# Optimization experiments

Measured on AMD Instinct MI355X. Metric: run time of the kernel, lower is better.

## Reference

```python
import jax, jax.numpy as jnp
from jax import lax
import numpy as np

EPS_COS = 1e-8   # cosine-similarity eps (matches F.cosine_similarity default scale)
EPS_IN = 1e-5    # InstanceNorm2d default eps
NEG = -1e9


def _conv3(x, w, b):
    # x: [B,C,H,W], w: [O,I,3,3]
    y = lax.conv_general_dilated(x, w, (1, 1), 'SAME',
                                 dimension_numbers=('NCHW', 'OIHW', 'NCHW'))
    return y + b[None, :, None, None]


def _inorm(x):
    m = jnp.mean(x, axis=(2, 3), keepdims=True)
    v = jnp.var(x, axis=(2, 3), keepdims=True)
    return (x - m) * lax.rsqrt(v + EPS_IN)


def _shift(former, latter, mask):
    # former/latter: [B,C,H,W]; mask: [H,W] int (1 = hole).
    # For every masked pixel, find the most cosine-similar UNMASKED pixel in the
    # latter (known-region encoder) features and copy the former feature from it.
    B, C, H, W = former.shape
    L = H * W
    lat = lax.stop_gradient(latter).reshape(B, C, L)           # attention is non-differentiable
    latn = lat / (jnp.linalg.norm(lat, axis=1, keepdims=True) + EPS_COS)
    sim = jnp.einsum('bcm,bcn->bmn', latn, latn)               # [B,L,L] query m -> key n
    mflat = mask.reshape(L) > 0
    sim = jnp.where(mflat[None, None, :], NEG, sim)            # keys must be unmasked
    idx = jnp.argmax(sim, axis=-1)                             # [B,L]
    fflat = former.reshape(B, C, L)
    gathered = jnp.take_along_axis(fflat, jnp.broadcast_to(idx[:, None, :], (B, C, L)), axis=2)
    shift = jnp.where(mflat[None, None, :], gathered, 0.0)     # zeros outside the hole
    return shift.reshape(B, C, H, W)


def setup_inputs() -> dict:
    key = jax.random.key(0)
    ks = jax.random.split(key, 6)
    B, C, H, W = 8, 256, 64, 64
    inp = jax.random.normal(ks[0], (B, 2 * C, H, W), dtype=jnp.float32)
    mask = jax.random.randint(ks[1], (H, W), 0, 2, dtype=jnp.int32)
    s1 = 1.0 / float(np.sqrt(2 * C * 9))
    s2 = 1.0 / float(np.sqrt(C * 9))
    W1 = jax.random.uniform(ks[2], (C, 2 * C, 3, 3), jnp.float32, -s1, s1)
    b1 = jax.random.uniform(ks[3], (C,), jnp.float32, -s1, s1)
    W2 = jax.random.uniform(ks[4], (C, C, 3, 3), jnp.float32, -s2, s2)
    b2 = jax.random.uniform(ks[5], (C,), jnp.float32, -s2, s2)
    return {"input": inp, "mask": mask, "W1": W1, "b1": b1, "W2": W2, "b2": b2}


def reference(input, mask, W1, b1, W2, b2):
    C = input.shape[1] // 2
    F_c = input[:, :C]          # former (decoder) features
    F_s = input[:, C:]          # latter (encoder) features
    F_shift = _shift(F_c, F_s, mask)
    F_fuse = F_c * F_shift
    F_com = jnp.concatenate([F_c, F_fuse], axis=1)             # [B,2C,H,W]
    h = jax.nn.relu(_inorm(_conv3(F_com, W1, b1)))
    res = _inorm(_conv3(h, W2, b2))
    return jnp.concatenate([F_c + res, F_s], axis=1)
```

## Files before the change

### kernel.cpp

```cpp
#include <hip/hip_runtime.h>
#include <hip/hip_bf16.h>
#include <math.h>

#define L 4096
#define C 256
#define B 8

typedef __attribute__((ext_vector_type(8))) short bf16x8;
typedef __attribute__((ext_vector_type(8))) ushort u16x8;
typedef __attribute__((ext_vector_type(4))) float f32x4;

__device__ inline ushort f2bu(float f) { __hip_bfloat16 h = __float2bfloat16(f); return *(ushort*)&h; }
__device__ inline float bu2f(ushort u) { __hip_bfloat16 h; *(ushort*)&h = u; return __bfloat162float(h); }

#define SWZ(c) ((((c) >> 1) & 3) << 4)

__global__ __launch_bounds__(256) void compact_mask(
    const int* __restrict__ mask, int* __restrict__ counts,
    int* __restrict__ maskedOrig, int* __restrict__ unmaskOrig,
    int* __restrict__ posOf)
{
    __shared__ int smM[256], smU[256];
    int t = threadIdx.x;
    int flags[16];
    int cm = 0, cu = 0;
    for (int k = 0; k < 16; ++k) {
        int l = t * 16 + k;
        int f = mask[l] > 0;
        flags[k] = f;
        cm += f; cu += !f;
    }
    smM[t] = cm; smU[t] = cu;
    __syncthreads();
    for (int off = 1; off < 256; off <<= 1) {
        int vM = 0, vU = 0;
        if (t >= off) { vM = smM[t - off]; vU = smU[t - off]; }
        __syncthreads();
        smM[t] += vM; smU[t] += vU;
        __syncthreads();
    }
    if (t == 255) { counts[0] = smM[255]; counts[1] = smU[255]; }
    int pm = smM[t] - cm, pu = smU[t] - cu;
    for (int k = 0; k < 16; ++k) {
        int l = t * 16 + k;
        if (flags[k]) { maskedOrig[pm] = l; posOf[l] = pm; pm++; }
        else          { unmaskOrig[pu] = l; posOf[l] = pu; pu++; }
    }
}

__global__ __launch_bounds__(256) void norm_transpose(
    const float* __restrict__ input, const int* __restrict__ mask,
    const int* __restrict__ counts, const int* __restrict__ posOf,
    ushort* __restrict__ fsnh, ushort* __restrict__ fsnl)
{
    int bx = blockIdx.x;
    int b = bx >> 7;
    int l0 = (bx & 127) * 32;
    __shared__ float tile[256 * 33];
    __shared__ float part[8 * 33];
    __shared__ float denom[32];
    __shared__ int   rowdst[32];
    int t = threadIdx.x;
    int lsub = t & 31, cg = t >> 5;
    for (int cc = 0; cc < 256; cc += 8) {
        int c = cc + cg;
        tile[c * 33 + lsub] = input[((size_t)(b * 512 + 256 + c)) * L + l0 + lsub];
    }
    __syncthreads();
    float s = 0.f;
    for (int c = cg; c < 256; c += 8) { float v = tile[c * 33 + lsub]; s = fmaf(v, v, s); }
    part[cg * 33 + lsub] = s;
    __syncthreads();
    if (t < 32) {
        float s2 = 0.f;
        for (int g = 0; g < 8; ++g) s2 += part[g * 33 + t];
        denom[t] = sqrtf(s2) + 1e-8f;
        int l = l0 + t;
        int Nm = counts[0];
        rowdst[t] = (mask[l] > 0) ? posOf[l] : (Nm + posOf[l]);
    }
    __syncthreads();
    for (int ls = 0; ls < 32; ++ls) {
        int r = rowdst[ls];
        float d = denom[ls];
        float val = tile[t * 33 + ls] / d;
        ushort h = f2bu(val);
        float hf = bu2f(h);
        ushort lo = f2bu(val - hf);
        size_t o = ((size_t)b * L + r) * C + t;
        fsnh[o] = h;
        fsnl[o] = lo;
    }
}

__global__ __launch_bounds__(256, 2) void sim_argmax_v8(
    const ushort* __restrict__ hi, const ushort* __restrict__ lo,
    const int* __restrict__ counts,
    float* __restrict__ pval, int* __restrict__ pidx)
{
    __shared__ ushort ldsB[32768];
    const int Nm = counts[0], Nu = counts[1];
    const int b = blockIdx.z;
    const int m0 = blockIdx.y * 64;
    const int half = blockIdx.x;
    const int t = threadIdx.x;
    const int w = t >> 6, l = t & 63;
    const int lm = l & 15, lk = l >> 4;
    const int key = lm << 4;

    const int nct = (Nu + 31) >> 5;
    const int hs = (nct + 1) >> 1;
    const int cA = half * hs, cB = half ? nct : hs;

    float bestv[4]; int bestn[4];
#pragma unroll
    for (int r = 0; r < 4; ++r) { bestv[r] = -3e38f; bestn[r] = 0; }

    if (m0 < Nm && cA < cB) {
        const char* bytesH = (const char*)hi;
        const char* bytesL = (const char*)lo;
        const size_t bL = (size_t)b * L;
        char* ldsc = (char*)ldsB;

#define STAGE(bofs, cc) do { \
    size_t gb = (bL + (size_t)Nm + (size_t)(cc) * 32) * 512; \
    _Pragma("unroll") \
    for (int i = 0; i < 4; ++i) { \
        int x = i * 4096 + t * 16; \
        int sx = x ^ (((x >> 9) & 15) << 4); \
        __builtin_amdgcn_global_load_lds((const __attribute__((address_space(1))) unsigned*)(bytesH + gb + sx), \
            (__attribute__((address_space(3))) unsigned*)(ldsc + (bofs) + x), 16, 0, 0); \
        __builtin_amdgcn_global_load_lds((const __attribute__((address_space(1))) unsigned*)(bytesL + gb + sx), \
            (__attribute__((address_space(3))) unsigned*)(ldsc + (bofs) + 16384 + x), 16, 0, 0); \
    } \
} while (0)

        STAGE(0, cA);
        if (cA + 1 < cB) STAGE(32768, cA + 1);

        const int rA = m0 + w * 16 + lm;
        bf16x8 ah[8], al[8];
        {
            const ushort* aH = hi + (bL + rA) * C + lk * 8;
            const ushort* aL = lo + (bL + rA) * C + lk * 8;
#pragma unroll
            for (int ks = 0; ks < 8; ++ks) {
                ah[ks] = *(const bf16x8*)(aH + ks * 32);
                al[ks] = *(const bf16x8*)(aL + ks * 32);
            }
        }

        for (int c = cA; c < cB; ++c) {
            int bob = ((c - cA) & 1) * 32768;
            if (c + 1 < cB) asm volatile("s_waitcnt vmcnt(8)" ::: "memory");
            else            asm volatile("s_waitcnt vmcnt(0)" ::: "memory");
            __builtin_amdgcn_s_barrier();
            const char* cbase = ldsc + bob;
            f32x4 acc[2];
            acc[0] = (f32x4){0.f, 0.f, 0.f, 0.f};
            acc[1] = (f32x4){0.f, 0.f, 0.f, 0.f};
#pragma unroll
            for (int ks = 0; ks < 8; ++ks) {
                bf16x8 bh[2], bl[2];
#pragma unroll
                for (int nf = 0; nf < 2; ++nf) {
                    int addr = (nf * 16 + lm) * 512 + ((ks * 64 + lk * 16) ^ key);
                    bh[nf] = *(const bf16x8*)(cbase + addr);
                    bl[nf] = *(const bf16x8*)(cbase + 16384 + addr);
                }
#pragma unroll
                for (int nf = 0; nf < 2; ++nf)
                    acc[nf] = __builtin_amdgcn_mfma_f32_16x16x32_bf16(ah[ks], bh[nf], acc[nf], 0, 0, 0);
#pragma unroll
                for (int nf = 0; nf < 2; ++nf)
                    acc[nf] = __builtin_amdgcn_mfma_f32_16x16x32_bf16(ah[ks], bl[nf], acc[nf], 0, 0, 0);
#pragma unroll
                for (int nf = 0; nf < 2; ++nf)
                    acc[nf] = __builtin_amdgcn_mfma_f32_16x16x32_bf16(al[ks], bh[nf], acc[nf], 0, 0, 0);
            }
            __builtin_amdgcn_s_barrier();
            if (c + 2 < cB) STAGE(bob, c + 2);
            int nbase = c * 32;
#pragma unroll
            for (int r = 0; r < 4; ++r) {
#pragma unroll
                for (int nf = 0; nf < 2; ++nf) {
                    int n = nbase + nf * 16 + lm;
                    float v = acc[nf][r];
                    if (n < Nu && v > bestv[r]) { bestv[r] = v; bestn[r] = n; }
                }
            }
        }
#undef STAGE
    }

    if (m0 >= Nm) return;
#pragma unroll
    for (int r = 0; r < 4; ++r) {
        float bv = bestv[r]; int bn = bestn[r];
#pragma unroll
        for (int mk = 1; mk < 16; mk <<= 1) {
            float ov = __shfl_xor(bv, mk, 64);
            int   on = __shfl_xor(bn, mk, 64);
            if (ov > bv || (ov == bv && on < bn)) { bv = ov; bn = on; }
        }
        if (lm == 0) {
            int m = m0 + w * 16 + lk * 4 + r;
            size_t o = ((size_t)(b * 4096 + m)) * 2 + half;
            pval[o] = bv; pidx[o] = bn;
        }
    }
}

__global__ __launch_bounds__(256) void wprep(
    const float* __restrict__ W1, const float* __restrict__ W2,
    ushort* __restrict__ W1bf, ushort* __restrict__ W2bf)
{
    int gid = blockIdx.x * 256 + threadIdx.x;
    const int N1 = 256 * 512 * 9;
    const int N2 = 256 * 256 * 9;
    if (gid < N1) {
        int ci = gid & 511; int rest = gid >> 9;
        int tau = rest % 9; int co = rest / 9;
        W1bf[gid] = f2bu(W1[((size_t)(co * 512 + ci)) * 9 + tau]);
    } else if (gid < N1 + N2) {
        int g = gid - N1;
        int ci = g & 255; int rest = g >> 8;
        int tau = rest % 9; int co = rest / 9;
        W2bf[g] = f2bu(W2[((size_t)(co * 256 + ci)) * 9 + tau]);
    }
}

__global__ __launch_bounds__(256) void in_prep1(
    const float* __restrict__ input, ushort* __restrict__ inT)
{
    int b = blockIdx.y;
    int p0 = blockIdx.x * 32;
    __shared__ float tile[256][33];
    int t = threadIdx.x;
    int pq = t & 7;
    for (int cc = 0; cc < 256; cc += 32) {
        int ci = cc + (t >> 3);
        float4 v = *(const float4*)(input + ((size_t)(b * 512 + ci)) * L + p0 + pq * 4);
        tile[ci][pq * 4 + 0] = v.x; tile[ci][pq * 4 + 1] = v.y;
        tile[ci][pq * 4 + 2] = v.z; tile[ci][pq * 4 + 3] = v.w;
    }
    __syncthreads();
    int c8 = t & 31;
    for (int pp = 0; pp < 32; pp += 8) {
        int pixloc = pp + (t >> 5);
        u16x8 u;
#pragma unroll
        for (int j = 0; j < 8; ++j) u[j] = f2bu(tile[c8 * 8 + j][pixloc]);
        *(u16x8*)(inT + ((size_t)(b * 4096 + p0 + pixloc)) * 512 + c8 * 8) = u;
    }
}

__global__ __launch_bounds__(256) void in_prep2(
    ushort* __restrict__ inT, const int* __restrict__ mask,
    const float* __restrict__ pval, const int* __restrict__ pidx,
    const int* __restrict__ posOf, const int* __restrict__ unmaskOrig)
{
    int gid = blockIdx.x * 256 + threadIdx.x;
    int c8 = gid & 31;
    int pix = (gid >> 5) & 4095;
    int b = gid >> 17;
    u16x8 out8;
    if (mask[pix] > 0) {
        int m = posOf[pix];
        size_t base = ((size_t)(b * 4096 + m)) * 2;
        float bv = pval[base]; int bn = pidx[base];
        float v1 = pval[base + 1]; int n1 = pidx[base + 1];
        if (v1 > bv || (v1 == bv && n1 < bn)) { bn = n1; }
        int n = unmaskOrig[bn];
        const ushort* rp = inT + ((size_t)(b * 4096 + pix)) * 512 + c8 * 8;
        const ushort* rn = inT + ((size_t)(b * 4096 + n)) * 512 + c8 * 8;
        u16x8 a = *(const u16x8*)rp;
        u16x8 bb = *(const u16x8*)rn;
#pragma unroll
        for (int j = 0; j < 8; ++j) out8[j] = f2bu(bu2f(a[j]) * bu2f(bb[j]));
    } else {
#pragma unroll
        for (int j = 0; j < 8; ++j) out8[j] = 0;
    }
    *(u16x8*)(inT + ((size_t)(b * 4096 + pix)) * 512 + 256 + c8 * 8) = out8;
}

template<int CKROW, int NORM_IN>
__global__ __launch_bounds__(256, 2) void conv_mfma(
    const ushort* __restrict__ Abf, const ushort* __restrict__ Wbf,
    const float* __restrict__ mrsIn,
    ushort* __restrict__ outH, float* __restrict__ psum)
{
    __shared__ float4 ldsv[62208 / 16];
    char* lds = (char*)ldsv;
    char* ldsB = lds + 25344;
    const int t = threadIdx.x;
    const int w = t >> 6;
    const int l = t & 63;
    const int lm = l & 15, lk = l >> 4;
    const int b = blockIdx.z;
    const int y0 = blockIdx.x * 4;
    const int c0 = blockIdx.y * 64;
    const int yw = y0 + w;
    const size_t abase = (size_t)b * 4096 * CKROW;

    f32x4 acc[4][4];
#pragma unroll
    for (int g = 0; g < 4; ++g)
#pragma unroll
        for (int nf = 0; nf < 4; ++nf) acc[g][nf] = (f32x4){0.f, 0.f, 0.f, 0.f};

    if (t < 48) {
        int r = t >> 3;
        int hX = ((t >> 2) & 1) ? 65 : 0;
        int hk = t & 3;
        *(float4*)(lds + (r * 66 + hX) * 64 + ((hk * 16) ^ SWZ(hX))) = (float4){0.f,0.f,0.f,0.f};
    }

    const int NKC = CKROW / 32;
    for (int kc = 0; kc < NKC; ++kc) {
        __syncthreads();
        {
            int x = t >> 2;
            int k8 = t & 3;
            int cX = x + 1;
            char* dbase = lds + cX * 64 + ((k8 * 16) ^ SWZ(cX));
            if (NORM_IN) {
                const float* mb = mrsIn + (size_t)b * 512 + (size_t)(kc * 32 + k8 * 8) * 2;
                float mm[8], rr[8];
#pragma unroll
                for (int j = 0; j < 8; ++j) { mm[j] = mb[2 * j]; rr[j] = mb[2 * j + 1]; }
#pragma unroll
                for (int r = 0; r < 6; ++r) {
                    int yy = y0 - 1 + r;
                    float4 ov = (float4){0.f, 0.f, 0.f, 0.f};
                    if (yy >= 0 && yy < 64) {
                        float4 v = *(const float4*)(Abf + abase + (size_t)(yy * 64 + x) * CKROW + kc * 32 + k8 * 8);
                        u16x8 u = *(u16x8*)&v;
                        u16x8 o;
#pragma unroll
                        for (int j = 0; j < 8; ++j) {
                            float z = (bu2f(u[j]) - mm[j]) * rr[j];
                            o[j] = f2bu(z > 0.f ? z : 0.f);
                        }
                        ov = *(float4*)&o;
                    }
                    *(float4*)(dbase + r * (66 * 64)) = ov;
                }
            } else {
#pragma unroll
                for (int r = 0; r < 6; ++r) {
                    int yy = y0 - 1 + r;
                    float4 v;
                    if (yy >= 0 && yy < 64)
                        v = *(const float4*)(Abf + abase + (size_t)(yy * 64 + x) * CKROW + kc * 32 + k8 * 8);
                    else
                        v = (float4){0.f, 0.f, 0.f, 0.f};
                    *(float4*)(dbase + r * (66 * 64)) = v;
                }
            }
            int cl = t >> 2;
            char* dbaseB = ldsB + cl * 64 + ((k8 * 16) ^ SWZ(cl));
            const ushort* sbase = Wbf + ((size_t)(c0 + cl) * 9) * CKROW + kc * 32 + k8 * 8;
#pragma unroll
            for (int tau = 0; tau < 9; ++tau) {
                *(float4*)(dbaseB + tau * (64 * 64)) = *(const float4*)(sbase + (size_t)tau * CKROW);
            }
        }
        __syncthreads();
#pragma unroll
        for (int ky = 0; ky < 3; ++ky) {
            int r = w + ky;
#pragma unroll
            for (int kx = 0; kx < 3; ++kx) {
                int tau = ky * 3 + kx;
                bf16x8 bfr[4];
#pragma unroll
                for (int nf = 0; nf < 4; ++nf) {
                    int cl = nf * 16 + lm;
                    bfr[nf] = *(bf16x8*)(ldsB + (tau * 64 + cl) * 64 + ((lk * 16) ^ SWZ(cl)));
                }
#pragma unroll
                for (int g = 0; g < 4; ++g) {
                    int aX = g * 16 + lm + kx;
                    bf16x8 afr = *(bf16x8*)(lds + (r * 66 + aX) * 64 + ((lk * 16) ^ SWZ(aX)));
#pragma unroll
                    for (int nf = 0; nf < 4; ++nf)
                        acc[g][nf] = __builtin_amdgcn_mfma_f32_16x16x32_bf16(afr, bfr[nf], acc[g][nf], 0, 0, 0);
                }
            }
        }
    }

#pragma unroll
    for (int g = 0; g < 4; ++g)
#pragma unroll
        for (int nf = 0; nf < 4; ++nf) {
            int cout = c0 + nf * 16 + lm;
#pragma unroll
            for (int r = 0; r < 4; ++r) {
                int pix = yw * 64 + g * 16 + lk * 4 + r;
                outH[((size_t)(b * 4096 + pix)) * 256 + cout] = f2bu(acc[g][nf][r]);
            }
        }

    float s[4], q[4];
#pragma unroll
    for (int nf = 0; nf < 4; ++nf) {
        float ss = 0.f, qq = 0.f;
#pragma unroll
        for (int g = 0; g < 4; ++g)
#pragma unroll
            for (int r = 0; r < 4; ++r) { float v = acc[g][nf][r]; ss += v; qq = fmaf(v, v, qq); }
        ss += __shfl_xor(ss, 16, 64); ss += __shfl_xor(ss, 32, 64);
        qq += __shfl_xor(qq, 16, 64); qq += __shfl_xor(qq, 32, 64);
        s[nf] = ss; q[nf] = qq;
    }
    __syncthreads();
    float* S = (float*)lds;
    float* Q = (float*)(lds + 1024);
    if (l < 16) {
#pragma unroll
        for (int nf = 0; nf < 4; ++nf) {
            S[w * 64 + nf * 16 + l] = s[nf];
            Q[w * 64 + nf * 16 + l] = q[nf];
        }
    }
    __syncthreads();
    if (t < 64) {
        float ts = 0.f, tq = 0.f;
#pragma unroll
        for (int w2 = 0; w2 < 4; ++w2) { ts += S[w2 * 64 + t]; tq += Q[w2 * 64 + t]; }
        size_t o = (((size_t)(b * 256 + c0 + t)) * 16 + blockIdx.x) * 2;
        psum[o] = ts; psum[o + 1] = tq;
    }
}

__global__ __launch_bounds__(256) void stats_reduce(
    const float* __restrict__ psum, float* __restrict__ mrs)
{
    int b = blockIdx.x;
    int c = threadIdx.x;
    float s = 0.f, q = 0.f;
    size_t base = ((size_t)(b * 256 + c)) * 16;
    for (int k = 0; k < 16; ++k) { s += psum[(base + k) * 2]; q += psum[(base + k) * 2 + 1]; }
    float mean = s * (1.f / 4096.f);
    float var = q * (1.f / 4096.f) - mean * mean;
    float rs = rsqrtf(var + 1e-5f);
    mrs[(b * 256 + c) * 2] = mean;
    mrs[(b * 256 + c) * 2 + 1] = rs;
}

__global__ __launch_bounds__(256) void finalize_fs(
    const ushort* __restrict__ resbf, const float* __restrict__ mrs,
    const float* __restrict__ input, float* __restrict__ out)
{
    __shared__ float tileT[256][33];
    int bx = blockIdx.x;
    int t = threadIdx.x;
    if (bx < 8192) {
        size_t i = (size_t)bx * 256 + t;
        size_t b = i >> 18;
        size_t r = i & 262143;
        size_t o = ((size_t)(b * 512 + 256)) * 1024 + r;
        ((float4*)out)[o] = ((const float4*)input)[o];
        return;
    }
    int fb = bx - 8192;
    int b = fb >> 7;
    int p0 = (fb & 127) * 32;
    int c8 = t & 31;
    for (int pp = 0; pp < 32; pp += 8) {
        int pixloc = pp + (t >> 5);
        u16x8 u = *(const u16x8*)(resbf + (((size_t)(b * 4096 + p0 + pixloc)) << 8) + c8 * 8);
#pragma unroll
        for (int j = 0; j < 8; ++j) tileT[c8 * 8 + j][pixloc] = bu2f(u[j]);
    }
    __syncthreads();
    int pq = t & 7;
    for (int cc = 0; cc < 256; cc += 32) {
        int c = cc + (t >> 3);
        float m = mrs[(b * 256 + c) * 2];
        float rs = mrs[(b * 256 + c) * 2 + 1];
        size_t off = ((size_t)(b * 512 + c)) * L + p0 + pq * 4;
        float4 f = *(const float4*)(input + off);
        float4 o;
        o.x = f.x + (tileT[c][pq * 4 + 0] - m) * rs;
        o.y = f.y + (tileT[c][pq * 4 + 1] - m) * rs;
        o.z = f.z + (tileT[c][pq * 4 + 2] - m) * rs;
        o.w = f.w + (tileT[c][pq * 4 + 3] - m) * rs;
        *(float4*)(out + off) = o;
    }
}

extern "C" void kernel_launch(void* const* d_in, const int* in_sizes, int n_in,
                              void* d_out, int out_size, void* d_ws, size_t ws_size,
                              hipStream_t stream) {
    const float* input = (const float*)d_in[0];
    const int*   mask  = (const int*)d_in[1];
    const float* W1    = (const float*)d_in[2];
    const float* W2    = (const float*)d_in[4];
    float* out = (float*)d_out;
    (void)in_sizes; (void)n_in; (void)out_size; (void)ws_size;

    char* ob = (char*)d_out;
    char* wp = (char*)d_ws;

    ushort* fsnh = (ushort*)ob;
    ushort* fsnl = (ushort*)(ob + 16777216);
    float*  pval = (float*)(ob + 33554432);
    int*    pidx = (int*)(ob + 37748736);
    ushort* inT  = (ushort*)ob;
    ushort* hraw = (ushort*)(ob + 33554432);

    ushort* resbf  = (ushort*)wp;
    ushort* W1bf   = (ushort*)(wp + 16777216);
    ushort* W2bf   = (ushort*)(wp + 19136512);
    float*  psum1  = (float*)(wp + 20316160);
    float*  psum2  = (float*)(wp + 20578304);
    float*  mrs1   = (float*)(wp + 20840448);
    float*  mrs2   = (float*)(wp + 20856832);
    int* counts     = (int*)(wp + 20873216);
    int* maskedOrig = counts + 4;
    int* unmaskOrig = maskedOrig + L;
    int* posOf      = unmaskOrig + L;

    compact_mask<<<1, 256, 0, stream>>>(mask, counts, maskedOrig, unmaskOrig, posOf);
    norm_transpose<<<1024, 256, 0, stream>>>(input, mask, counts, posOf, fsnh, fsnl);
    sim_argmax_v8<<<dim3(2, 64, 8), 256, 0, stream>>>(fsnh, fsnl, counts, pval, pidx);
    wprep<<<6912, 256, 0, stream>>>(W1, W2, W1bf, W2bf);
    in_prep1<<<dim3(128, 8), 256, 0, stream>>>(input, inT);
    in_prep2<<<4096, 256, 0, stream>>>(inT, mask, pval, pidx, posOf, unmaskOrig);
    conv_mfma<512, 0><<<dim3(16, 4, 8), 256, 0, stream>>>(inT, W1bf, (const float*)nullptr, hraw, psum1);
    stats_reduce<<<8, 256, 0, stream>>>(psum1, mrs1);
    conv_mfma<256, 1><<<dim3(16, 4, 8), 256, 0, stream>>>(hraw, W2bf, mrs1, resbf, psum2);
    stats_reduce<<<8, 256, 0, stream>>>(psum2, mrs2);
    finalize_fs<<<9216, 256, 0, stream>>>(resbf, mrs2, input, out);
}
```

Baseline: 270.3 us.

## Split sim-argmax key range four ways and drop LDS double buffering

The similarity/argmax kernel now divides the unmasked key tiles among four blocks per query tile instead of two, which doubles the grid. LDS use is halved by replacing the double-buffered prefetch with a single buffer that is synchronously waited on each iteration. The merge in in_prep2 now reduces four partial results. The goal is more occupancy and parallelism, but the loss of overlap between loads and MFMA could stall each block, and the partial buffers get more writes and reads.

```diff
diff --git a/kernel.cpp b/kernel.cpp
--- a/kernel.cpp
+++ b/kernel.cpp
@@ -93,24 +93,24 @@
     }
 }
 
-__global__ __launch_bounds__(256, 2) void sim_argmax_v8(
+__global__ __launch_bounds__(256, 2) void sim_argmax_v9(
     const ushort* __restrict__ hi, const ushort* __restrict__ lo,
     const int* __restrict__ counts,
     float* __restrict__ pval, int* __restrict__ pidx)
 {
-    __shared__ ushort ldsB[32768];
+    __shared__ ushort ldsB[16384];
     const int Nm = counts[0], Nu = counts[1];
     const int b = blockIdx.z;
     const int m0 = blockIdx.y * 64;
-    const int half = blockIdx.x;
+    const int nq = blockIdx.x;
     const int t = threadIdx.x;
     const int w = t >> 6, l = t & 63;
     const int lm = l & 15, lk = l >> 4;
     const int key = lm << 4;
 
     const int nct = (Nu + 31) >> 5;
-    const int hs = (nct + 1) >> 1;
-    const int cA = half * hs, cB = half ? nct : hs;
+    const int cA = (nq * nct) >> 2;
+    const int cB = ((nq + 1) * nct) >> 2;
 
     float bestv[4]; int bestn[4];
 #pragma unroll
@@ -122,21 +122,20 @@
         const size_t bL = (size_t)b * L;
         char* ldsc = (char*)ldsB;
 
-#define STAGE(bofs, cc) do { \
+#define STAGE(cc) do { \
     size_t gb = (bL + (size_t)Nm + (size_t)(cc) * 32) * 512; \
     _Pragma("unroll") \
     for (int i = 0; i < 4; ++i) { \
         int x = i * 4096 + t * 16; \
         int sx = x ^ (((x >> 9) & 15) << 4); \
         __builtin_amdgcn_global_load_lds((const __attribute__((address_space(1))) unsigned*)(bytesH + gb + sx), \
-            (__attribute__((address_space(3))) unsigned*)(ldsc + (bofs) + x), 16, 0, 0); \
+            (__attribute__((address_space(3))) unsigned*)(ldsc + x), 16, 0, 0); \
         __builtin_amdgcn_global_load_lds((const __attribute__((address_space(1))) unsigned*)(bytesL + gb + sx), \
-            (__attribute__((address_space(3))) unsigned*)(ldsc + (bofs) + 16384 + x), 16, 0, 0); \
+            (__attribute__((address_space(3))) unsigned*)(ldsc + 16384 + x), 16, 0, 0); \
     } \
 } while (0)
 
-        STAGE(0, cA);
-        if (cA + 1 < cB) STAGE(32768, cA + 1);
+        STAGE(cA);
 
         const int rA = m0 + w * 16 + lm;
         bf16x8 ah[8], al[8];
@@ -151,11 +150,8 @@
         }
 
         for (int c = cA; c < cB; ++c) {
-            int bob = ((c - cA) & 1) * 32768;
-            if (c + 1 < cB) asm volatile("s_waitcnt vmcnt(8)" ::: "memory");
-            else            asm volatile("s_waitcnt vmcnt(0)" ::: "memory");
-            __builtin_amdgcn_s_barrier();
-            const char* cbase = ldsc + bob;
+            asm volatile("s_waitcnt vmcnt(0)" ::: "memory");
+            __syncthreads();
             f32x4 acc[2];
             acc[0] = (f32x4){0.f, 0.f, 0.f, 0.f};
             acc[1] = (f32x4){0.f, 0.f, 0.f, 0.f};
@@ -165,8 +161,8 @@
 #pragma unroll
                 for (int nf = 0; nf < 2; ++nf) {
                     int addr = (nf * 16 + lm) * 512 + ((ks * 64 + lk * 16) ^ key);
-                    bh[nf] = *(const bf16x8*)(cbase + addr);
-                    bl[nf] = *(const bf16x8*)(cbase + 16384 + addr);
+                    bh[nf] = *(const bf16x8*)(ldsc + addr);
+                    bl[nf] = *(const bf16x8*)(ldsc + 16384 + addr);
                 }
 #pragma unroll
                 for (int nf = 0; nf < 2; ++nf)
@@ -178,8 +174,8 @@
                 for (int nf = 0; nf < 2; ++nf)
                     acc[nf] = __builtin_amdgcn_mfma_f32_16x16x32_bf16(al[ks], bh[nf], acc[nf], 0, 0, 0);
             }
-            __builtin_amdgcn_s_barrier();
-            if (c + 2 < cB) STAGE(bob, c + 2);
+            __syncthreads();
+            if (c + 1 < cB) STAGE(c + 1);
             int nbase = c * 32;
 #pragma unroll
             for (int r = 0; r < 4; ++r) {
@@ -206,7 +202,7 @@
         }
         if (lm == 0) {
             int m = m0 + w * 16 + lk * 4 + r;
-            size_t o = ((size_t)(b * 4096 + m)) * 2 + half;
+            size_t o = ((size_t)(b * 4096 + m)) * 4 + nq;
             pval[o] = bv; pidx[o] = bn;
         }
     }
@@ -268,10 +264,13 @@
     u16x8 out8;
     if (mask[pix] > 0) {
         int m = posOf[pix];
-        size_t base = ((size_t)(b * 4096 + m)) * 2;
+        size_t base = ((size_t)(b * 4096 + m)) * 4;
         float bv = pval[base]; int bn = pidx[base];
-        float v1 = pval[base + 1]; int n1 = pidx[base + 1];
-        if (v1 > bv || (v1 == bv && n1 < bn)) { bn = n1; }
+#pragma unroll
+        for (int p = 1; p < 4; ++p) {
+            float v = pval[base + p]; int n2 = pidx[base + p];
+            if (v > bv || (v == bv && n2 < bn)) { bv = v; bn = n2; }
+        }
         int n = unmaskOrig[bn];
         const ushort* rp = inT + ((size_t)(b * 4096 + pix)) * 512 + c8 * 8;
         const ushort* rn = inT + ((size_t)(b * 4096 + n)) * 512 + c8 * 8;
@@ -528,7 +527,7 @@
 
     compact_mask<<<1, 256, 0, stream>>>(mask, counts, maskedOrig, unmaskOrig, posOf);
     norm_transpose<<<1024, 256, 0, stream>>>(input, mask, counts, posOf, fsnh, fsnl);
-    sim_argmax_v8<<<dim3(2, 64, 8), 256, 0, stream>>>(fsnh, fsnl, counts, pval, pidx);
+    sim_argmax_v9<<<dim3(4, 64, 8), 256, 0, stream>>>(fsnh, fsnl, counts, pval, pidx);
     wprep<<<6912, 256, 0, stream>>>(W1, W2, W1bf, W2bf);
     in_prep1<<<dim3(128, 8), 256, 0, stream>>>(input, inT);
     in_prep2<<<4096, 256, 0, stream>>>(inT, mask, pval, pidx, posOf, unmaskOrig);
```

Measured after the change: 249.9 us, median of 2. 1.08x faster.
